# Kernel optimization log

Measured on AMD Instinct MI355X. Metric: run time of the kernel, lower is better.

Reference implementation:

```python
import jax, jax.numpy as jnp
import numpy as np

B, CIN, H, W = 16, 3, 112, 112
S, D, C, NC = 3, 4, 128, 100   # num_scales, depth, channels, num_classes
THRESH = 0.9
WSCALE = 0.05  # keep activations numerically sane through relu-conv cascade


def _conv3x3(x, w, b):
    # x: [B,Cin,H,W], w: [Cout,Cin,3,3]
    y = jax.lax.conv_general_dilated(
        x, w, window_strides=(1, 1), padding='SAME',
        dimension_numbers=('NCHW', 'OIHW', 'NCHW'))
    return y + b[None, :, None, None]


def setup_inputs() -> dict:
    key = jax.random.key(0)
    k = jax.random.split(key, 7)
    return {
        'x': jax.random.normal(k[0], (B, CIN, H, W), jnp.float32),
        'init_w': jax.random.normal(k[1], (S, C, CIN, 3, 3), jnp.float32) * WSCALE,
        'init_b': jax.random.normal(k[2], (S, C), jnp.float32) * WSCALE,
        'block_w': jax.random.normal(k[3], (D, S, C, C, 3, 3), jnp.float32) * WSCALE,
        'block_b': jax.random.normal(k[4], (D, S, C), jnp.float32) * WSCALE,
        'cls_w': jax.random.normal(k[5], (D, NC, C), jnp.float32) * WSCALE,
        'cls_b': jax.random.normal(k[6], (D, NC), jnp.float32) * WSCALE,
    }


def reference(x, init_w, init_b, block_w, block_b, cls_w, cls_b):
    # init blocks: one conv per scale (no activation, as in source)
    feats = [_conv3x3(x, init_w[s], init_b[s]) for s in range(S)]

    outputs = jnp.zeros((x.shape[0], cls_w.shape[1]), x.dtype)
    exited = jnp.zeros((x.shape[0],), jnp.bool_)

    # exit_layers = [0..D-1], so classifier index == block index
    for i in range(D):
        feats = [jax.nn.relu(_conv3x3(feats[s], block_w[i, s], block_b[i, s]))
                 for s in range(S)]
        pooled = feats[-1].mean(axis=(2, 3))              # [B, C]
        logits = pooled @ cls_w[i].T + cls_b[i]           # [B, NC]
        conf = jnp.max(jax.nn.softmax(logits, axis=-1), axis=-1)
        take = jnp.logical_and(~exited, conf >= THRESH)   # vectorized early-exit
        outputs = jnp.where(take[:, None], logits, outputs)
        exited = jnp.logical_or(exited, take)

    # samples that never exited get the last classifier's logits
    final_logits = feats[-1].mean(axis=(2, 3)) @ cls_w[-1].T + cls_b[-1]
    outputs = jnp.where(exited[:, None], outputs, final_logits)
    return outputs
```

## Files before the change

### kernel.cpp

```cpp
#include <hip/hip_runtime.h>
#include <hip/hip_bf16.h>


typedef unsigned int uint;
typedef unsigned short u16;
typedef __bf16 bf16x8 __attribute__((ext_vector_type(8)));
typedef short short8 __attribute__((ext_vector_type(8)));
typedef unsigned short ushort8 __attribute__((ext_vector_type(8)));
typedef float f32x4 __attribute__((ext_vector_type(4)));

#define NB   16
#define CCH  128
#define NCLS 100
#define HW   12544
#define NTILE 98

__device__ __forceinline__ u16 f2bf(float f) {
    uint u = __float_as_uint(f);
    return (u16)((u + 0x7fffu + ((u >> 16) & 1u)) >> 16);
}

__global__ __launch_bounds__(256) void convert_w(
    const float* __restrict__ bw, u16* __restrict__ wb)
{
    int idx = blockIdx.x * 256 + threadIdx.x;
    if (idx >= 4 * 9 * 16384) return;
    int d = idx / 147456, r = idx % 147456;
    int t = r / 16384, r2 = r & 16383;
    int co = r2 >> 7, ci = r2 & 127;
    float v = bw[((size_t)(d * 3 + 2) * 16384 + co * 128 + ci) * 9 + t];
    wb[idx] = f2bf(v);
}

__global__ __launch_bounds__(256) void conv_init(
    const float* __restrict__ in,
    const float* __restrict__ wgt,
    const float* __restrict__ bias,
    u16* __restrict__ outp)
{
    const int tile = blockIdx.x;
    const int cg   = blockIdx.y;
    const int n    = blockIdx.z;
    const int h0 = (tile / 7) * 16, w0 = (tile % 7) * 16;
    const int tid = threadIdx.x;
    const int sid = tid & 63, wv = tid >> 6;
    const int tx = sid & 7, ty = sid >> 3;

    __shared__ float s_in[3][18][18];
    __shared__ float s_w[3][9][32];

    float acc[2][2][8];
    #pragma unroll
    for (int a = 0; a < 2; a++)
        #pragma unroll
        for (int b = 0; b < 2; b++)
            #pragma unroll
            for (int c = 0; c < 8; c++) acc[a][b][c] = 0.f;

    const float* in_n = in + (size_t)n * 3 * HW;
    const int cbase = cg * 32;

    for (int e = tid; e < 3 * 324; e += 256) {
        int ck = e / 324, p = e % 324;
        int y = p / 18, x = p % 18;
        int gh = h0 + y - 1, gw = w0 + x - 1;
        float v = 0.f;
        if ((unsigned)gh < 112u && (unsigned)gw < 112u)
            v = in_n[(size_t)ck * HW + gh * 112 + gw];
        s_in[ck][y][x] = v;
    }
    for (int e = tid; e < 3 * 9 * 32; e += 256) {
        int co = e / 27, r = e % 27;
        int ck = r / 9, kidx = r % 9;
        s_w[ck][kidx][co] = wgt[((size_t)(cbase + co) * 3 + ck) * 9 + kidx];
    }
    __syncthreads();

    #pragma unroll
    for (int ck = 0; ck < 3; ck++) {
        float rowv[4][4];
        #pragma unroll
        for (int r = 0; r < 4; r++) {
            float2 a  = *(const float2*)&s_in[ck][ty * 2 + r][tx * 2];
            float2 b2 = *(const float2*)&s_in[ck][ty * 2 + r][tx * 2 + 2];
            rowv[r][0] = a.x; rowv[r][1] = a.y;
            rowv[r][2] = b2.x; rowv[r][3] = b2.y;
        }
        #pragma unroll
        for (int kh = 0; kh < 3; kh++)
            #pragma unroll
            for (int kw = 0; kw < 3; kw++) {
                float i00 = rowv[kh][kw],     i01 = rowv[kh][kw + 1];
                float i10 = rowv[kh + 1][kw], i11 = rowv[kh + 1][kw + 1];
                const float* wp = &s_w[ck][kh * 3 + kw][wv * 8];
                #pragma unroll
                for (int co = 0; co < 8; co++) {
                    float wval = wp[co];
                    acc[0][0][co] += i00 * wval;
                    acc[0][1][co] += i01 * wval;
                    acc[1][0][co] += i10 * wval;
                    acc[1][1][co] += i11 * wval;
                }
            }
    }

    float bv[8];
    #pragma unroll
    for (int co = 0; co < 8; co++) bv[co] = bias[cbase + wv * 8 + co];
    #pragma unroll
    for (int dy = 0; dy < 2; dy++)
        #pragma unroll
        for (int dx = 0; dx < 2; dx++) {
            ushort8 pk;
            #pragma unroll
            for (int co = 0; co < 8; co++)
                pk[co] = f2bf(acc[dy][dx][co] + bv[co]);
            int h = h0 + ty * 2 + dy, w = w0 + tx * 2 + dx;
            *(ushort8*)(outp + (((size_t)n * HW + h * 112 + w) << 7) + cbase + wv * 8) = pk;
        }
}

#define AS 40

template<bool STORE>
__global__ __launch_bounds__(256, 3) void conv_mfma(
    const u16* __restrict__ in,
    const u16* __restrict__ wb,
    const float* __restrict__ bias,
    u16* __restrict__ outp,
    float* __restrict__ partial)
{
    __shared__ u16 s_in[180 * AS];
    __shared__ u16 s_w[4][128 * 32];
    float* s_pool = (float*)s_in;

    const int tile = blockIdx.x;
    const int n    = blockIdx.y;
    const int h0 = (tile / 7) * 8, w0 = (tile % 7) * 16;
    const int tid = threadIdx.x, lane = tid & 63;
    const int wid = tid >> 6, wm = wid >> 1, wn = wid & 1;
    const int l15 = lane & 15, l4 = lane >> 4;

    const u16* in_n = in + ((size_t)n * HW << 7);

    const int co0 = tid >> 2;
    const int g0  = (tid & 3) ^ ((tid >> 3) & 3);
    const int k0  = g0 << 3;
    const int wp0 = (tid & 3) << 3;

    #pragma unroll
    for (int s01 = 0; s01 < 2; ++s01) {
        const u16* src = wb + s01 * 16384;
        uint4 va = *(const uint4*)(src + (co0 << 7) + k0);
        uint4 vb = *(const uint4*)(src + ((co0 + 64) << 7) + k0);
        *(uint4*)(&s_w[s01][co0 * 32] + wp0) = va;
        *(uint4*)(&s_w[s01][(co0 + 64) * 32] + wp0) = vb;
    }
    uint4 wA0, wA1, wB0, wB1;
    {
        const u16* s2 = wb + 2 * 16384;
        const u16* s3 = wb + 3 * 16384;
        wA0 = *(const uint4*)(s2 + (co0 << 7) + k0);
        wA1 = *(const uint4*)(s2 + ((co0 + 64) << 7) + k0);
        wB0 = *(const uint4*)(s3 + (co0 << 7) + k0);
        wB1 = *(const uint4*)(s3 + ((co0 + 64) << 7) + k0);
    }

    #pragma unroll
    for (int r2 = 0; r2 < 3; ++r2) {
        int g = tid + (r2 << 8);
        if (g < 720) {
            int px = g >> 2, c8 = (g & 3) << 3;
            int hh = px / 18, ww2 = px - hh * 18;
            int gh = h0 + hh - 1, gw = w0 + ww2 - 1;
            uint4 v = make_uint4(0, 0, 0, 0);
            if ((unsigned)gh < 112u && (unsigned)gw < 112u)
                v = *(const uint4*)(in_n + ((size_t)(gh * 112 + gw) << 7) + c8);
            *(uint4*)(s_in + px * AS + c8) = v;
        }
    }

    f32x4 acc[4][4];
    #pragma unroll
    for (int i = 0; i < 4; ++i)
        #pragma unroll
        for (int j = 0; j < 4; ++j)
            #pragma unroll
            for (int e = 0; e < 4; ++e) acc[i][j][e] = 0.f;

    int a_base[4], b_base[4];
    #pragma unroll
    for (int fi = 0; fi < 4; ++fi) a_base[fi] = (wm * 4 + fi) * 18 + l15;
    #pragma unroll
    for (int nj = 0; nj < 4; ++nj)
        b_base[nj] = (wn * 64 + nj * 16 + l15) * 32 + ((l4 ^ ((l15 >> 1) & 3)) << 3);

    __syncthreads();

    #pragma unroll
    for (int P = 0; P < 18; ++P) {
        const int s0 = 2 * P, s1 = 2 * P + 1;

        {
            const int t = s0 % 9, kh = t / 3, kw = t - kh * 3;
            bf16x8 a[4], b[4];
            #pragma unroll
            for (int fi = 0; fi < 4; ++fi) {
                const u16* p = s_in + (a_base[fi] + kh * 18 + kw) * AS + (l4 << 3);
                a[fi] = __builtin_bit_cast(bf16x8, *(const short8*)p);
            }
            const u16* rb = &s_w[s0 & 3][0];
            #pragma unroll
            for (int nj = 0; nj < 4; ++nj)
                b[nj] = __builtin_bit_cast(bf16x8, *(const short8*)(rb + b_base[nj]));

            uint4 nA0, nA1;
            if (s0 + 4 < 36) {
                const u16* srcn = wb + ((s0 + 4) % 9) * 16384 + ((s0 + 4) / 9) * 32;
                nA0 = *(const uint4*)(srcn + (co0 << 7) + k0);
                nA1 = *(const uint4*)(srcn + ((co0 + 64) << 7) + k0);
            }

            #pragma unroll
            for (int fi = 0; fi < 4; ++fi)
                #pragma unroll
                for (int nj = 0; nj < 4; ++nj)
                    acc[fi][nj] = __builtin_amdgcn_mfma_f32_16x16x32_bf16(
                        a[fi], b[nj], acc[fi][nj], 0, 0, 0);

            if (s0 + 2 < 36) {
                u16* wd = &s_w[(s0 + 2) & 3][0];
                *(uint4*)(wd + co0 * 32 + wp0) = wA0;
                *(uint4*)(wd + (co0 + 64) * 32 + wp0) = wA1;
            }
            if (s0 + 4 < 36) { wA0 = nA0; wA1 = nA1; }
        }

        if (s0 % 9 == 8) {
            const int qn = s0 / 9 + 1;
            asm volatile("s_waitcnt lgkmcnt(0)" ::: "memory");
            __builtin_amdgcn_s_barrier();
            #pragma unroll
            for (int r2 = 0; r2 < 3; ++r2) {
                int g = tid + (r2 << 8);
                if (g < 720) {
                    int px = g >> 2, c8 = (g & 3) << 3;
                    int hh = px / 18, ww2 = px - hh * 18;
                    int gh = h0 + hh - 1, gw = w0 + ww2 - 1;
                    uint4 v = make_uint4(0, 0, 0, 0);
                    if ((unsigned)gh < 112u && (unsigned)gw < 112u)
                        v = *(const uint4*)(in_n + ((size_t)(gh * 112 + gw) << 7)
                                            + (qn << 5) + c8);
                    *(uint4*)(s_in + px * AS + c8) = v;
                }
            }
            asm volatile("s_waitcnt lgkmcnt(0)" ::: "memory");
            __builtin_amdgcn_s_barrier();
            __builtin_amdgcn_sched_barrier(0);
        }

        {
            const int t = s1 % 9, kh = t / 3, kw = t - kh * 3;
            bf16x8 a[4], b[4];
            #pragma unroll
            for (int fi = 0; fi < 4; ++fi) {
                const u16* p = s_in + (a_base[fi] + kh * 18 + kw) * AS + (l4 << 3);
                a[fi] = __builtin_bit_cast(bf16x8, *(const short8*)p);
            }
            const u16* rb = &s_w[s1 & 3][0];
            #pragma unroll
            for (int nj = 0; nj < 4; ++nj)
                b[nj] = __builtin_bit_cast(bf16x8, *(const short8*)(rb + b_base[nj]));

            uint4 nB0, nB1;
            if (s1 + 4 < 36) {
                const u16* srcn = wb + ((s1 + 4) % 9) * 16384 + ((s1 + 4) / 9) * 32;
                nB0 = *(const uint4*)(srcn + (co0 << 7) + k0);
                nB1 = *(const uint4*)(srcn + ((co0 + 64) << 7) + k0);
            }

            #pragma unroll
            for (int fi = 0; fi < 4; ++fi)
                #pragma unroll
                for (int nj = 0; nj < 4; ++nj)
                    acc[fi][nj] = __builtin_amdgcn_mfma_f32_16x16x32_bf16(
                        a[fi], b[nj], acc[fi][nj], 0, 0, 0);

            if (s1 + 2 < 36) {
                u16* wd = &s_w[(s1 + 2) & 3][0];
                *(uint4*)(wd + co0 * 32 + wp0) = wB0;
                *(uint4*)(wd + (co0 + 64) * 32 + wp0) = wB1;
            }
            if (s1 + 4 < 36) { wB0 = nB0; wB1 = nB1; }
        }

        asm volatile("s_waitcnt lgkmcnt(0)" ::: "memory");
        __builtin_amdgcn_s_barrier();
        __builtin_amdgcn_sched_barrier(0);

        if (s1 % 9 == 8 && s1 != 35) {
            const int qn = s1 / 9 + 1;
            #pragma unroll
            for (int r2 = 0; r2 < 3; ++r2) {
                int g = tid + (r2 << 8);
                if (g < 720) {
                    int px = g >> 2, c8 = (g & 3) << 3;
                    int hh = px / 18, ww2 = px - hh * 18;
                    int gh = h0 + hh - 1, gw = w0 + ww2 - 1;
                    uint4 v = make_uint4(0, 0, 0, 0);
                    if ((unsigned)gh < 112u && (unsigned)gw < 112u)
                        v = *(const uint4*)(in_n + ((size_t)(gh * 112 + gw) << 7)
                                            + (qn << 5) + c8);
                    *(uint4*)(s_in + px * AS + c8) = v;
                }
            }
            asm volatile("s_waitcnt lgkmcnt(0)" ::: "memory");
            __builtin_amdgcn_s_barrier();
            __builtin_amdgcn_sched_barrier(0);
        }
    }

    float bv[4], ps[4];
    #pragma unroll
    for (int nj = 0; nj < 4; ++nj) { bv[nj] = bias[wn * 64 + nj * 16 + l15]; ps[nj] = 0.f; }
    u16* out_n = outp + ((size_t)n * HW << 7);
    #pragma unroll
    for (int fi = 0; fi < 4; ++fi) {
        int h = h0 + wm * 4 + fi;
        #pragma unroll
        for (int j = 0; j < 4; ++j) {
            int w = w0 + (l4 << 2) + j;
            u16* pr = out_n + ((size_t)(h * 112 + w) << 7);
            #pragma unroll
            for (int nj = 0; nj < 4; ++nj) {
                float v = fmaxf(acc[fi][nj][j] + bv[nj], 0.f);
                ps[nj] += v;
                if (STORE) pr[wn * 64 + nj * 16 + l15] = f2bf(v);
            }
        }
    }
    #pragma unroll
    for (int nj = 0; nj < 4; ++nj) {
        ps[nj] += __shfl_xor(ps[nj], 16, 64);
        ps[nj] += __shfl_xor(ps[nj], 32, 64);
    }
    __syncthreads();
    if (l4 == 0) {
        #pragma unroll
        for (int nj = 0; nj < 4; ++nj)
            s_pool[wm * 128 + wn * 64 + nj * 16 + l15] = ps[nj];
    }
    __syncthreads();
    if (tid < 128)
        partial[((size_t)n * NTILE + tile) * 128 + tid] = s_pool[tid] + s_pool[128 + tid];
}

__global__ __launch_bounds__(128) void logits_k(
    const float* __restrict__ partial,
    const float* __restrict__ cw,
    const float* __restrict__ cb,
    float* __restrict__ lg)
{
    const int i = blockIdx.x, n = blockIdx.y;
    const int tid = threadIdx.x;
    __shared__ float pool[128];
    const float* pp = partial + ((size_t)(i * NB + n) * NTILE) * 128;
    float s = 0.f;
    for (int t = 0; t < NTILE; ++t) s += pp[t * 128 + tid];
    pool[tid] = s * (1.f / HW);
    __syncthreads();
    if (tid < NCLS) {
        const float* wp = cw + ((size_t)i * NCLS + tid) * CCH;
        float a = cb[i * NCLS + tid];
        #pragma unroll
        for (int c = 0; c < CCH; c += 4) {
            float4 w4 = *(const float4*)(wp + c);
            a += pool[c] * w4.x + pool[c + 1] * w4.y
               + pool[c + 2] * w4.z + pool[c + 3] * w4.w;
        }
        lg[(i * NB + n) * NCLS + tid] = a;
    }
}

__global__ __launch_bounds__(256) void select_k(
    const float* __restrict__ lg,
    float* __restrict__ out)
{
    __shared__ float slg[4 * NB * NCLS];
    __shared__ int chosen[NB];
    const int tid = threadIdx.x;
    for (int e = tid; e < 4 * NB * NCLS; e += 256) slg[e] = lg[e];
    __syncthreads();
    if (tid < NB) {
        int n = tid, ch = 3;
        for (int i = 0; i < 3; i++) {
            const float* row = &slg[(i * NB + n) * NCLS];
            float m = -1e30f;
            for (int j = 0; j < NCLS; j++) m = fmaxf(m, row[j]);
            float se = 0.f;
            for (int j = 0; j < NCLS; j++) se += expf(row[j] - m);
            if (1.f / se >= 0.9f) { ch = i; break; }
        }
        chosen[n] = ch;
    }
    __syncthreads();
    for (int e = tid; e < NB * NCLS; e += 256) {
        int n = e / NCLS, j = e % NCLS;
        out[e] = slg[(chosen[n] * NB + n) * NCLS + j];
    }
}

extern "C" void kernel_launch(void* const* d_in, const int* in_sizes, int n_in,
                              void* d_out, int out_size, void* d_ws, size_t ws_size,
                              hipStream_t stream) {
    const float* x       = (const float*)d_in[0];
    const float* init_w  = (const float*)d_in[1];
    const float* init_b  = (const float*)d_in[2];
    const float* block_w = (const float*)d_in[3];
    const float* block_b = (const float*)d_in[4];
    const float* cls_w   = (const float*)d_in[5];
    const float* cls_b   = (const float*)d_in[6];
    float* out = (float*)d_out;

    char* ws = (char*)d_ws;
    u16* fA        = (u16*)ws;
    u16* fB        = (u16*)(ws + 51380224);
    u16* wb        = (u16*)(ws + 102760448);
    float* partial = (float*)(ws + 103940096);
    float* lgbuf   = (float*)(ws + 107151360);

    convert_w<<<2304, 256, 0, stream>>>(block_w, wb);
    conv_init<<<dim3(49, 4, NB), 256, 0, stream>>>(
        x, init_w + 2 * 128 * 27, init_b + 2 * 128, fA);

    u16* cur = fA;
    u16* nxt = fB;
    for (int i = 0; i < 4; ++i) {
        if (i < 3)
            conv_mfma<true><<<dim3(NTILE, NB), 256, 0, stream>>>(
                cur, wb + (size_t)i * 147456, block_b + (i * 3 + 2) * 128, nxt,
                partial + (size_t)i * NB * NTILE * 128);
        else
            conv_mfma<false><<<dim3(NTILE, NB), 256, 0, stream>>>(
                cur, wb + (size_t)i * 147456, block_b + (i * 3 + 2) * 128, nxt,
                partial + (size_t)i * NB * NTILE * 128);
        u16* t = cur; cur = nxt; nxt = t;
    }

    logits_k<<<dim3(4, NB), 128, 0, stream>>>(partial, cls_w, cls_b, lgbuf);
    select_k<<<1, 256, 0, stream>>>(lgbuf, out);
}
```

Baseline: 327.3 us.

## Pre-swizzle weight slices and stream them to LDS via direct global_load_lds

The weight conversion kernel now writes each 128x32 slice already in the XOR-swizzled LDS layout, so each wave can copy contiguous 16-byte chunks. The conv kernel then uses global_load_lds (async global-to-LDS) two steps ahead instead of staging weights through registers and ds_write. This removes register pressure and LDS write instructions from the MFMA loop. It changes the per-step wait from an lgkmcnt wait to a vmcnt(0) wait, which also waits for any in-flight global loads and may expose latency.

```diff
diff --git a/kernel.cpp b/kernel.cpp
--- a/kernel.cpp
+++ b/kernel.cpp
@@ -20,16 +20,25 @@
     return (u16)((u + 0x7fffu + ((u >> 16) & 1u)) >> 16);
 }
 
+__device__ __forceinline__ void gload16(const u16* g, u16* l) {
+    __builtin_amdgcn_global_load_lds(
+        (const __attribute__((address_space(1))) uint*)g,
+        (__attribute__((address_space(3))) uint*)l, 16, 0, 0);
+}
+
 __global__ __launch_bounds__(256) void convert_w(
-    const float* __restrict__ bw, u16* __restrict__ wb)
+    const float* __restrict__ bw, u16* __restrict__ wbs)
 {
     int idx = blockIdx.x * 256 + threadIdx.x;
-    if (idx >= 4 * 9 * 16384) return;
+    if (idx >= 4 * 147456) return;
     int d = idx / 147456, r = idx % 147456;
-    int t = r / 16384, r2 = r & 16383;
-    int co = r2 >> 7, ci = r2 & 127;
-    float v = bw[((size_t)(d * 3 + 2) * 16384 + co * 128 + ci) * 9 + t];
-    wb[idx] = f2bf(v);
+    int s = r >> 12;
+    int p = r & 4095;
+    int co = p >> 5, gpos = (p >> 3) & 3, e = p & 7;
+    int q = s / 9, t = s % 9;
+    int cin = q * 32 + ((gpos ^ ((co >> 1) & 3)) << 3) + e;
+    float v = bw[(((size_t)(d * 3 + 2) * 128 + co) * 128 + cin) * 9 + t];
+    wbs[idx] = f2bf(v);
 }
 
 __global__ __launch_bounds__(256) void conv_init(
@@ -125,13 +134,13 @@
 template<bool STORE>
 __global__ __launch_bounds__(256, 3) void conv_mfma(
     const u16* __restrict__ in,
-    const u16* __restrict__ wb,
+    const u16* __restrict__ wbs,
     const float* __restrict__ bias,
     u16* __restrict__ outp,
     float* __restrict__ partial)
 {
     __shared__ u16 s_in[180 * AS];
-    __shared__ u16 s_w[4][128 * 32];
+    __shared__ u16 s_w[4][4096];
     float* s_pool = (float*)s_in;
 
     const int tile = blockIdx.x;
@@ -143,27 +152,15 @@
 
     const u16* in_n = in + ((size_t)n * HW << 7);
 
-    const int co0 = tid >> 2;
-    const int g0  = (tid & 3) ^ ((tid >> 3) & 3);
-    const int k0  = g0 << 3;
-    const int wp0 = (tid & 3) << 3;
+    const u16* wsrc_base = wbs + wid * 1024 + (lane << 3);
+    u16* wdst_base = &s_w[0][0] + wid * 1024;
 
     #pragma unroll
     for (int s01 = 0; s01 < 2; ++s01) {
-        const u16* src = wb + s01 * 16384;
-        uint4 va = *(const uint4*)(src + (co0 << 7) + k0);
-        uint4 vb = *(const uint4*)(src + ((co0 + 64) << 7) + k0);
-        *(uint4*)(&s_w[s01][co0 * 32] + wp0) = va;
-        *(uint4*)(&s_w[s01][(co0 + 64) * 32] + wp0) = vb;
-    }
-    uint4 wA0, wA1, wB0, wB1;
-    {
-        const u16* s2 = wb + 2 * 16384;
-        const u16* s3 = wb + 3 * 16384;
-        wA0 = *(const uint4*)(s2 + (co0 << 7) + k0);
-        wA1 = *(const uint4*)(s2 + ((co0 + 64) << 7) + k0);
-        wB0 = *(const uint4*)(s3 + (co0 << 7) + k0);
-        wB1 = *(const uint4*)(s3 + ((co0 + 64) << 7) + k0);
+        const u16* src = wsrc_base + (s01 << 12);
+        u16* dst = wdst_base + (s01 << 12);
+        gload16(src, dst);
+        gload16(src + 512, dst + 512);
     }
 
     #pragma unroll
@@ -201,6 +198,17 @@
     for (int P = 0; P < 18; ++P) {
         const int s0 = 2 * P, s1 = 2 * P + 1;
 
+        #pragma unroll
+        for (int d2 = 2; d2 < 4; ++d2) {
+            const int sp = s0 + d2;
+            if (sp < 36) {
+                const u16* src = wsrc_base + (sp << 12);
+                u16* dst = wdst_base + ((sp & 3) << 12);
+                gload16(src, dst);
+                gload16(src + 512, dst + 512);
+            }
+        }
+
         {
             const int t = s0 % 9, kh = t / 3, kw = t - kh * 3;
             bf16x8 a[4], b[4];
@@ -213,27 +221,12 @@
             #pragma unroll
             for (int nj = 0; nj < 4; ++nj)
                 b[nj] = __builtin_bit_cast(bf16x8, *(const short8*)(rb + b_base[nj]));
-
-            uint4 nA0, nA1;
-            if (s0 + 4 < 36) {
-                const u16* srcn = wb + ((s0 + 4) % 9) * 16384 + ((s0 + 4) / 9) * 32;
-                nA0 = *(const uint4*)(srcn + (co0 << 7) + k0);
-                nA1 = *(const uint4*)(srcn + ((co0 + 64) << 7) + k0);
-            }
-
             #pragma unroll
             for (int fi = 0; fi < 4; ++fi)
                 #pragma unroll
                 for (int nj = 0; nj < 4; ++nj)
                     acc[fi][nj] = __builtin_amdgcn_mfma_f32_16x16x32_bf16(
                         a[fi], b[nj], acc[fi][nj], 0, 0, 0);
-
-            if (s0 + 2 < 36) {
-                u16* wd = &s_w[(s0 + 2) & 3][0];
-                *(uint4*)(wd + co0 * 32 + wp0) = wA0;
-                *(uint4*)(wd + (co0 + 64) * 32 + wp0) = wA1;
-            }
-            if (s0 + 4 < 36) { wA0 = nA0; wA1 = nA1; }
         }
 
         if (s0 % 9 == 8) {
@@ -271,30 +264,15 @@
             #pragma unroll
             for (int nj = 0; nj < 4; ++nj)
                 b[nj] = __builtin_bit_cast(bf16x8, *(const short8*)(rb + b_base[nj]));
-
-            uint4 nB0, nB1;
-            if (s1 + 4 < 36) {
-                const u16* srcn = wb + ((s1 + 4) % 9) * 16384 + ((s1 + 4) / 9) * 32;
-                nB0 = *(const uint4*)(srcn + (co0 << 7) + k0);
-                nB1 = *(const uint4*)(srcn + ((co0 + 64) << 7) + k0);
-            }
-
             #pragma unroll
             for (int fi = 0; fi < 4; ++fi)
                 #pragma unroll
                 for (int nj = 0; nj < 4; ++nj)
                     acc[fi][nj] = __builtin_amdgcn_mfma_f32_16x16x32_bf16(
                         a[fi], b[nj], acc[fi][nj], 0, 0, 0);
-
-            if (s1 + 2 < 36) {
-                u16* wd = &s_w[(s1 + 2) & 3][0];
-                *(uint4*)(wd + co0 * 32 + wp0) = wB0;
-                *(uint4*)(wd + (co0 + 64) * 32 + wp0) = wB1;
-            }
-            if (s1 + 4 < 36) { wB0 = nB0; wB1 = nB1; }
-        }
-
-        asm volatile("s_waitcnt lgkmcnt(0)" ::: "memory");
+        }
+
+        asm volatile("s_waitcnt vmcnt(0)" ::: "memory");
         __builtin_amdgcn_s_barrier();
         __builtin_amdgcn_sched_barrier(0);
 
@@ -425,11 +403,11 @@
     char* ws = (char*)d_ws;
     u16* fA        = (u16*)ws;
     u16* fB        = (u16*)(ws + 51380224);
-    u16* wb        = (u16*)(ws + 102760448);
+    u16* wbs       = (u16*)(ws + 102760448);
     float* partial = (float*)(ws + 103940096);
     float* lgbuf   = (float*)(ws + 107151360);
 
-    convert_w<<<2304, 256, 0, stream>>>(block_w, wb);
+    convert_w<<<2304, 256, 0, stream>>>(block_w, wbs);
     conv_init<<<dim3(49, 4, NB), 256, 0, stream>>>(
         x, init_w + 2 * 128 * 27, init_b + 2 * 128, fA);
 
@@ -438,11 +416,11 @@
     for (int i = 0; i < 4; ++i) {
         if (i < 3)
             conv_mfma<true><<<dim3(NTILE, NB), 256, 0, stream>>>(
-                cur, wb + (size_t)i * 147456, block_b + (i * 3 + 2) * 128, nxt,
+                cur, wbs + (size_t)i * 147456, block_b + (i * 3 + 2) * 128, nxt,
                 partial + (size_t)i * NB * NTILE * 128);
         else
             conv_mfma<false><<<dim3(NTILE, NB), 256, 0, stream>>>(
-                cur, wb + (size_t)i * 147456, block_b + (i * 3 + 2) * 128, nxt,
+                cur, wbs + (size_t)i * 147456, block_b + (i * 3 + 2) * 128, nxt,
                 partial + (size_t)i * NB * NTILE * 128);
         u16* t = cur; cur = nxt; nxt = t;
     }
```

Measured after the change: 315.6 us. 1.04x faster.
